# Optimization experiments

Measured on AMD Instinct MI355X. Metric: run time of the kernel, lower is better.

Reference implementation:

```python
import jax, jax.numpy as jnp
import numpy as np

B, M, N, DIM = 4, 3, 2048, 512
H = 4
HD = DIM // H  # 128
SCALE = float(np.sqrt(HD))  # code divides scores by sqrt(head_dim)


def setup_inputs() -> dict:
    key = jax.random.key(0)
    ks = jax.random.split(key, 9)
    s = 0.02
    return {
        "query": jax.random.normal(ks[0], (B, M, N, DIM), jnp.float32),
        "key": jax.random.normal(ks[1], (B, M, N, DIM), jnp.float32),
        "value": jax.random.normal(ks[2], (B, M, N, DIM), jnp.float32),
        "Wq": jax.random.normal(ks[3], (DIM, DIM), jnp.float32) * s,
        "bq": jax.random.normal(ks[4], (DIM,), jnp.float32) * s,
        "Wk": jax.random.normal(ks[5], (DIM, DIM), jnp.float32) * s,
        "bk": jax.random.normal(ks[6], (DIM,), jnp.float32) * s,
        "Wv": jax.random.normal(ks[7], (DIM, DIM), jnp.float32) * s,
        "bv": jax.random.normal(ks[8], (DIM,), jnp.float32) * s,
    }


def reference(query, key, value, Wq, bq, Wk, bk, Wv, bv):
    b, m, n, dim = query.shape
    # nn.Linear: x @ W.T + b
    Q = (query @ Wq.T + bq).reshape(b, m, n, H, HD)
    K = (key @ Wk.T + bk).reshape(b, m, n, H, HD)
    V = (value @ Wv.T + bv).reshape(b, m, n, H, HD)
    # scores: [b, m, H, n, n]
    scores = jnp.einsum("bmqhd,bmkhd->bmhqk", Q, K) / SCALE
    attn = jax.nn.softmax(scores, axis=-1)
    out = jnp.einsum("bmhqk,bmkhd->bmqhd", attn, V)
    return out.reshape(b, m, n, dim)
```

## Files before the change

kernel.cpp:

```cpp
#include <hip/hip_runtime.h>
#include <hip/hip_bf16.h>


typedef short s16x8 __attribute__((ext_vector_type(8)));
typedef unsigned short u16x8 __attribute__((ext_vector_type(8)));
typedef float f32x4 __attribute__((ext_vector_type(4)));

#define MFMA16(a, b, c) __builtin_amdgcn_mfma_f32_16x16x32_bf16((a), (b), (c), 0, 0, 0)

static __device__ __forceinline__ unsigned short f2bf(float f) {
    union { float f; unsigned u; } v; v.f = f;
    unsigned r = v.u + 0x7FFFu + ((v.u >> 16) & 1u);
    return (unsigned short)(r >> 16);
}
static __device__ __forceinline__ unsigned pk2(float a, float b) {
    unsigned r;
    asm("v_cvt_pk_bf16_f32 %0, %1, %2" : "=v"(r) : "v"(a), "v"(b));
    return r;
}

#define OSTR 72

__global__ __launch_bounds__(256, 2)
void qkv_proj_kernel(const float* __restrict__ Xq, const float* __restrict__ Xk,
                     const float* __restrict__ Xv,
                     const float* __restrict__ Wq, const float* __restrict__ bq,
                     const float* __restrict__ Wk, const float* __restrict__ bk,
                     const float* __restrict__ Wv, const float* __restrict__ bv,
                     unsigned short* __restrict__ ws_q,
                     unsigned short* __restrict__ ws_k,
                     unsigned short* __restrict__ ws_vt)
{
    __shared__ __align__(16) char smem[65536];

    const int which = blockIdx.z;
    const float* X    = (which == 0) ? Xq : (which == 1) ? Xk : Xv;
    const float* W    = (which == 0) ? Wq : (which == 1) ? Wk : Wv;
    const float* bias = (which == 0) ? bq : (which == 1) ? bk : bv;

    const int r0 = blockIdx.x * 128;
    const int c0 = blockIdx.y * 128;
    const int tid = threadIdx.x;
    const int lane = tid & 63, wave = tid >> 6;
    const int l15 = lane & 15, quad = lane >> 4;
    const int wr = (wave >> 1) * 64, wc = (wave & 1) * 64;

    const int srow = tid >> 4;
    const int scol = tid & 15;
    const int cf = scol * 4;
    const int cb = scol * 8;

    f32x4 acc[4][4] = {};

    {
        char* A0 = smem;
        char* B0 = smem + 16384;
        for (int i = 0; i < 8; ++i) {
            const int row = i * 16 + srow;
            float4 fa = *(const float4*)&X[(size_t)(r0 + row) * 512 + cf];
            float4 fb = *(const float4*)&W[(size_t)(c0 + row) * 512 + cf];
            uint2 wa, wb;
            wa.x = pk2(fa.x, fa.y); wa.y = pk2(fa.z, fa.w);
            wb.x = pk2(fb.x, fb.y); wb.y = pk2(fb.z, fb.w);
            const int sw = cb ^ ((row & 7) << 4);
            *(uint2*)(A0 + row * 128 + sw) = wa;
            *(uint2*)(B0 + row * 128 + sw) = wb;
        }
    }
    __syncthreads();

    for (int it = 0; it < 8; ++it) {
        char* Ac = smem + (it & 1) * 32768;
        char* Bc = Ac + 16384;
        const bool pre = (it < 7);

        float4 ra[8], rb[8];
        if (pre) {
            const int kn = (it + 1) * 64;
            for (int i = 0; i < 8; ++i) {
                const int row = i * 16 + srow;
                ra[i] = *(const float4*)&X[(size_t)(r0 + row) * 512 + kn + cf];
                rb[i] = *(const float4*)&W[(size_t)(c0 + row) * 512 + kn + cf];
            }
        }

        for (int kk = 0; kk < 2; ++kk) {
            s16x8 af[4], bf_[4];
            for (int mi = 0; mi < 4; ++mi) {
                const int row = wr + mi * 16 + l15;
                af[mi] = *(const s16x8*)(Ac + row * 128 +
                                         ((kk * 64 + quad * 16) ^ ((row & 7) << 4)));
            }
            for (int ni = 0; ni < 4; ++ni) {
                const int row = wc + ni * 16 + l15;
                bf_[ni] = *(const s16x8*)(Bc + row * 128 +
                                          ((kk * 64 + quad * 16) ^ ((row & 7) << 4)));
            }
            for (int mi = 0; mi < 4; ++mi)
                for (int ni = 0; ni < 4; ++ni)
                    acc[mi][ni] = MFMA16(af[mi], bf_[ni], acc[mi][ni]);
        }

        if (pre) {
            char* An = smem + ((it & 1) ^ 1) * 32768;
            char* Bn = An + 16384;
            for (int i = 0; i < 8; ++i) {
                const int row = i * 16 + srow;
                uint2 wa, wb;
                wa.x = pk2(ra[i].x, ra[i].y); wa.y = pk2(ra[i].z, ra[i].w);
                wb.x = pk2(rb[i].x, rb[i].y); wb.y = pk2(rb[i].z, rb[i].w);
                const int sw = cb ^ ((row & 7) << 4);
                *(uint2*)(An + row * 128 + sw) = wa;
                *(uint2*)(Bn + row * 128 + sw) = wb;
            }
        }
        __syncthreads();
    }

    float bvals[4];
    for (int ni = 0; ni < 4; ++ni) bvals[ni] = bias[c0 + wc + ni * 16 + l15];

    __syncthreads();
    unsigned short* St = (unsigned short*)smem + wave * (64 * OSTR);
    const int h = blockIdx.y;
    const int bm = (r0 + wr) >> 11;
    const int n0 = (r0 + wr) & 2047;

    if (which != 2) {
        for (int mi = 0; mi < 4; ++mi)
            for (int ni = 0; ni < 4; ++ni)
                for (int r = 0; r < 4; ++r)
                    St[(mi * 16 + quad * 4 + r) * OSTR + ni * 16 + l15] =
                        f2bf(acc[mi][ni][r] + bvals[ni]);
        unsigned short* dst = (which == 0) ? ws_q : ws_k;
        for (int p = 0; p < 8; ++p) {
            const int row = p * 8 + (lane >> 3);
            const int coff = (lane & 7) * 8;
            s16x8 v = *(const s16x8*)&St[row * OSTR + coff];
            *(s16x8*)&dst[((size_t)(bm * 4 + h) * 2048 + n0 + row) * 128 + wc + coff] = v;
        }
    } else {
        for (int mi = 0; mi < 4; ++mi)
            for (int ni = 0; ni < 4; ++ni)
                for (int r = 0; r < 4; ++r)
                    St[(ni * 16 + l15) * OSTR + mi * 16 + quad * 4 + r] =
                        f2bf(acc[mi][ni][r] + bvals[ni]);
        for (int p = 0; p < 8; ++p) {
            const int col = p * 8 + (lane >> 3);
            const int roff = (lane & 7) * 8;
            s16x8 v = *(const s16x8*)&St[col * OSTR + roff];
            *(s16x8*)&ws_vt[(((size_t)(bm * 4 + h)) * 128 + wc + col) * 2048 + n0 + roff] = v;
        }
    }
}

#define KSTR 272
#define VSTR 80
#define PQST 80

__global__ __launch_bounds__(256)
void attn_kernel(const unsigned short* __restrict__ Qw,
                 const unsigned short* __restrict__ Kw,
                 const unsigned short* __restrict__ Vtw,
                 float* __restrict__ out)
{
    __shared__ char lds[48128];
    char* Kb0 = lds;
    char* Kb1 = lds + 8704;
    char* Vb0 = lds + 17408;
    char* Vb1 = lds + 27648;
    char* Pb  = lds + 37888;

    const int tid = threadIdx.x, lane = tid & 63, wave = tid >> 6;
    const int l15 = lane & 15, quad = lane >> 4;
    const int q0 = blockIdx.x * 128, h = blockIdx.y, bm = blockIdx.z;

    const unsigned short* Qh = Qw  + (size_t)(bm * 4 + h) * 2048 * 128;
    const unsigned short* Kh = Kw  + (size_t)(bm * 4 + h) * 2048 * 128;
    const unsigned short* Vh = Vtw + (size_t)(bm * 4 + h) * 128 * 2048;

    const int sk_key  = tid >> 3, sk_c   = tid & 7;
    const int sv_hd   = tid >> 1, sv_hlf = tid & 1;

    s16x8 qf[2][4];
    for (int qh = 0; qh < 2; ++qh)
        for (int kk = 0; kk < 4; ++kk)
            qf[qh][kk] = *(const s16x8*)&Qh[(size_t)(q0 + wave * 32 + qh * 16 + l15) * 128 + kk * 32 + quad * 8];

    {
        u16x8 ka = *(const u16x8*)&Kh[(size_t)sk_key * 128 + sk_c * 16];
        u16x8 kb = *(const u16x8*)&Kh[(size_t)sk_key * 128 + sk_c * 16 + 8];
        u16x8 va = *(const u16x8*)&Vh[(size_t)sv_hd * 2048 + sv_hlf * 16];
        u16x8 vb = *(const u16x8*)&Vh[(size_t)sv_hd * 2048 + sv_hlf * 16 + 8];
        *(u16x8*)(Kb0 + sk_key * KSTR + sk_c * 32)      = ka;
        *(u16x8*)(Kb0 + sk_key * KSTR + sk_c * 32 + 16) = kb;
        *(u16x8*)(Vb0 + sv_hd * VSTR + sv_hlf * 32)      = va;
        *(u16x8*)(Vb0 + sv_hd * VSTR + sv_hlf * 32 + 16) = vb;
    }
    __syncthreads();

    f32x4 acc[2][8] = {};
    float rsum[2] = {0.f, 0.f};
    char* Pw = Pb + wave * 2560;

    const float CEXP = 1.4426950408889634f / 11.313708498984761f;

    for (int it = 0; it < 64; ++it) {
        const int k0 = it * 32;
        char* Kc = (it & 1) ? Kb1 : Kb0;
        char* Vc = (it & 1) ? Vb1 : Vb0;
        char* Kn = (it & 1) ? Kb0 : Kb1;
        char* Vn = (it & 1) ? Vb0 : Vb1;
        const bool do_stage = (it < 63);

        u16x8 ka, kb, va, vb;
        if (do_stage) {
            const int kn0 = k0 + 32;
            ka = *(const u16x8*)&Kh[(size_t)(kn0 + sk_key) * 128 + sk_c * 16];
            kb = *(const u16x8*)&Kh[(size_t)(kn0 + sk_key) * 128 + sk_c * 16 + 8];
            va = *(const u16x8*)&Vh[(size_t)sv_hd * 2048 + kn0 + sv_hlf * 16];
            vb = *(const u16x8*)&Vh[(size_t)sv_hd * 2048 + kn0 + sv_hlf * 16 + 8];
        }

        f32x4 s[2][2] = {};
        __builtin_amdgcn_s_setprio(1);
        for (int kk = 0; kk < 4; ++kk) {
            s16x8 kf0 = *(const s16x8*)(Kc + (l15)      * KSTR + (kk * 4 + quad) * 16);
            s16x8 kf1 = *(const s16x8*)(Kc + (16 + l15) * KSTR + (kk * 4 + quad) * 16);
            s[0][0] = MFMA16(kf0, qf[0][kk], s[0][0]);
            s[0][1] = MFMA16(kf1, qf[0][kk], s[0][1]);
            s[1][0] = MFMA16(kf0, qf[1][kk], s[1][0]);
            s[1][1] = MFMA16(kf1, qf[1][kk], s[1][1]);
        }
        __builtin_amdgcn_s_setprio(0);

        if (do_stage) {
            *(u16x8*)(Kn + sk_key * KSTR + sk_c * 32)      = ka;
            *(u16x8*)(Kn + sk_key * KSTR + sk_c * 32 + 16) = kb;
            *(u16x8*)(Vn + sv_hd * VSTR + sv_hlf * 32)      = va;
            *(u16x8*)(Vn + sv_hd * VSTR + sv_hlf * 32 + 16) = vb;
        }

        for (int qh = 0; qh < 2; ++qh)
            for (int ni = 0; ni < 2; ++ni) {
                const float p0 = exp2f(s[qh][ni][0] * CEXP);
                const float p1 = exp2f(s[qh][ni][1] * CEXP);
                const float p2 = exp2f(s[qh][ni][2] * CEXP);
                const float p3 = exp2f(s[qh][ni][3] * CEXP);
                rsum[qh] += (p0 + p1) + (p2 + p3);
                uint2 w; w.x = pk2(p0, p1); w.y = pk2(p2, p3);
                *(uint2*)(Pw + (qh * 16 + l15) * PQST + ni * 32 + quad * 8) = w;
            }

        s16x8 pf0 = *(const s16x8*)(Pw + (l15)      * PQST + quad * 16);
        s16x8 pf1 = *(const s16x8*)(Pw + (16 + l15) * PQST + quad * 16);
        __builtin_amdgcn_s_setprio(1);
        for (int mb = 0; mb < 8; ++mb) {
            s16x8 vtf = *(const s16x8*)(Vc + (mb * 16 + l15) * VSTR + quad * 16);
            acc[0][mb] = MFMA16(vtf, pf0, acc[0][mb]);
            acc[1][mb] = MFMA16(vtf, pf1, acc[1][mb]);
        }
        __builtin_amdgcn_s_setprio(0);

        __syncthreads();
    }

    for (int qh = 0; qh < 2; ++qh) {
        rsum[qh] += __shfl_xor(rsum[qh], 16);
        rsum[qh] += __shfl_xor(rsum[qh], 32);
    }
    for (int qh = 0; qh < 2; ++qh) {
        const float inv = 1.f / rsum[qh];
        float* orow = out + ((size_t)bm * 2048 + q0 + wave * 32 + qh * 16 + l15) * 512 + h * 128;
        for (int mb = 0; mb < 8; ++mb) {
            float4 v;
            v.x = acc[qh][mb][0] * inv; v.y = acc[qh][mb][1] * inv;
            v.z = acc[qh][mb][2] * inv; v.w = acc[qh][mb][3] * inv;
            *(float4*)&orow[mb * 16 + quad * 4] = v;
        }
    }
}

extern "C" void kernel_launch(void* const* d_in, const int* in_sizes, int n_in,
                              void* d_out, int out_size, void* d_ws, size_t ws_size,
                              hipStream_t stream) {
    const float* Xq = (const float*)d_in[0];
    const float* Xk = (const float*)d_in[1];
    const float* Xv = (const float*)d_in[2];
    const float* Wq = (const float*)d_in[3];
    const float* bq = (const float*)d_in[4];
    const float* Wk = (const float*)d_in[5];
    const float* bk = (const float*)d_in[6];
    const float* Wv = (const float*)d_in[7];
    const float* bv = (const float*)d_in[8];
    float* out = (float*)d_out;

    unsigned short* ws = (unsigned short*)d_ws;
    const size_t per_tensor = (size_t)12 * 4 * 2048 * 128;
    unsigned short* ws_q  = ws;
    unsigned short* ws_k  = ws + per_tensor;
    unsigned short* ws_vt = ws + 2 * per_tensor;

    qkv_proj_kernel<<<dim3(192, 4, 3), 256, 0, stream>>>(
        Xq, Xk, Xv, Wq, bq, Wk, bk, Wv, bv, ws_q, ws_k, ws_vt);

    attn_kernel<<<dim3(16, 4, 12), 256, 0, stream>>>(ws_q, ws_k, ws_vt, out);
}
```

Measured before the change: 447.4 us.

## Keep P in registers via permlane swaps, XOR-swizzle K in LDS, use hardware exp

Removes the per-wave LDS round trip for the probability tile. P is now packed into MFMA operand layout in registers using v_permlane32/16_swap, which saves LDS writes and reads and the LDS space they used. The padded K stride is replaced by an XOR swizzle to avoid bank conflicts without padding, and exp2f is replaced by raw v_exp_f32. The next-tile LDS stores move after the PV MFMAs, which delays them. The risks are that the permlane lane mapping must match the MFMA operand layout exactly, and that v_exp_f32 does no range handling.

```diff
diff --git a/kernel.cpp b/kernel.cpp
--- a/kernel.cpp
+++ b/kernel.cpp
@@ -16,6 +16,11 @@
 static __device__ __forceinline__ unsigned pk2(float a, float b) {
     unsigned r;
     asm("v_cvt_pk_bf16_f32 %0, %1, %2" : "=v"(r) : "v"(a), "v"(b));
+    return r;
+}
+static __device__ __forceinline__ float exp2_hw(float x) {
+    float r;
+    asm("v_exp_f32 %0, %1" : "=v"(r) : "v"(x));
     return r;
 }
 
@@ -154,9 +159,7 @@
     }
 }
 
-#define KSTR 272
 #define VSTR 80
-#define PQST 80
 
 __global__ __launch_bounds__(256)
 void attn_kernel(const unsigned short* __restrict__ Qw,
@@ -164,12 +167,11 @@
                  const unsigned short* __restrict__ Vtw,
                  float* __restrict__ out)
 {
-    __shared__ char lds[48128];
+    __shared__ char lds[36864];
     char* Kb0 = lds;
-    char* Kb1 = lds + 8704;
-    char* Vb0 = lds + 17408;
-    char* Vb1 = lds + 27648;
-    char* Pb  = lds + 37888;
+    char* Kb1 = lds + 8192;
+    char* Vb0 = lds + 16384;
+    char* Vb1 = lds + 26624;
 
     const int tid = threadIdx.x, lane = tid & 63, wave = tid >> 6;
     const int l15 = lane & 15, quad = lane >> 4;
@@ -181,6 +183,8 @@
 
     const int sk_key  = tid >> 3, sk_c   = tid & 7;
     const int sv_hd   = tid >> 1, sv_hlf = tid & 1;
+    const int skx = sk_key & 7;
+    const int krx = (l15 & 7) << 4;
 
     s16x8 qf[2][4];
     for (int qh = 0; qh < 2; ++qh)
@@ -192,8 +196,8 @@
         u16x8 kb = *(const u16x8*)&Kh[(size_t)sk_key * 128 + sk_c * 16 + 8];
         u16x8 va = *(const u16x8*)&Vh[(size_t)sv_hd * 2048 + sv_hlf * 16];
         u16x8 vb = *(const u16x8*)&Vh[(size_t)sv_hd * 2048 + sv_hlf * 16 + 8];
-        *(u16x8*)(Kb0 + sk_key * KSTR + sk_c * 32)      = ka;
-        *(u16x8*)(Kb0 + sk_key * KSTR + sk_c * 32 + 16) = kb;
+        *(u16x8*)(Kb0 + sk_key * 256 + (((sk_c * 2) ^ skx) << 4))     = ka;
+        *(u16x8*)(Kb0 + sk_key * 256 + (((sk_c * 2 + 1) ^ skx) << 4)) = kb;
         *(u16x8*)(Vb0 + sv_hd * VSTR + sv_hlf * 32)      = va;
         *(u16x8*)(Vb0 + sv_hd * VSTR + sv_hlf * 32 + 16) = vb;
     }
@@ -201,7 +205,6 @@
 
     f32x4 acc[2][8] = {};
     float rsum[2] = {0.f, 0.f};
-    char* Pw = Pb + wave * 2560;
 
     const float CEXP = 1.4426950408889634f / 11.313708498984761f;
 
@@ -225,8 +228,8 @@
         f32x4 s[2][2] = {};
         __builtin_amdgcn_s_setprio(1);
         for (int kk = 0; kk < 4; ++kk) {
-            s16x8 kf0 = *(const s16x8*)(Kc + (l15)      * KSTR + (kk * 4 + quad) * 16);
-            s16x8 kf1 = *(const s16x8*)(Kc + (16 + l15) * KSTR + (kk * 4 + quad) * 16);
+            s16x8 kf0 = *(const s16x8*)(Kc + l15 * 256        + (((kk * 4 + quad) << 4) ^ krx));
+            s16x8 kf1 = *(const s16x8*)(Kc + (16 + l15) * 256 + (((kk * 4 + quad) << 4) ^ krx));
             s[0][0] = MFMA16(kf0, qf[0][kk], s[0][0]);
             s[0][1] = MFMA16(kf1, qf[0][kk], s[0][1]);
             s[1][0] = MFMA16(kf0, qf[1][kk], s[1][0]);
@@ -234,33 +237,42 @@
         }
         __builtin_amdgcn_s_setprio(0);
 
-        if (do_stage) {
-            *(u16x8*)(Kn + sk_key * KSTR + sk_c * 32)      = ka;
-            *(u16x8*)(Kn + sk_key * KSTR + sk_c * 32 + 16) = kb;
-            *(u16x8*)(Vn + sv_hd * VSTR + sv_hlf * 32)      = va;
-            *(u16x8*)(Vn + sv_hd * VSTR + sv_hlf * 32 + 16) = vb;
-        }
-
-        for (int qh = 0; qh < 2; ++qh)
-            for (int ni = 0; ni < 2; ++ni) {
-                const float p0 = exp2f(s[qh][ni][0] * CEXP);
-                const float p1 = exp2f(s[qh][ni][1] * CEXP);
-                const float p2 = exp2f(s[qh][ni][2] * CEXP);
-                const float p3 = exp2f(s[qh][ni][3] * CEXP);
-                rsum[qh] += (p0 + p1) + (p2 + p3);
-                uint2 w; w.x = pk2(p0, p1); w.y = pk2(p2, p3);
-                *(uint2*)(Pw + (qh * 16 + l15) * PQST + ni * 32 + quad * 8) = w;
-            }
-
-        s16x8 pf0 = *(const s16x8*)(Pw + (l15)      * PQST + quad * 16);
-        s16x8 pf1 = *(const s16x8*)(Pw + (16 + l15) * PQST + quad * 16);
+        s16x8 pf[2];
+        for (int qh = 0; qh < 2; ++qh) {
+            const float p00 = exp2_hw(s[qh][0][0] * CEXP);
+            const float p01 = exp2_hw(s[qh][0][1] * CEXP);
+            const float p02 = exp2_hw(s[qh][0][2] * CEXP);
+            const float p03 = exp2_hw(s[qh][0][3] * CEXP);
+            const float p10 = exp2_hw(s[qh][1][0] * CEXP);
+            const float p11 = exp2_hw(s[qh][1][1] * CEXP);
+            const float p12 = exp2_hw(s[qh][1][2] * CEXP);
+            const float p13 = exp2_hw(s[qh][1][3] * CEXP);
+            rsum[qh] += ((p00 + p01) + (p02 + p03)) + ((p10 + p11) + (p12 + p13));
+            unsigned x0 = pk2(p00, p01), y0 = pk2(p02, p03);
+            unsigned x1 = pk2(p10, p11), y1 = pk2(p12, p13);
+            asm("v_permlane32_swap_b32 %0, %1" : "+v"(x0), "+v"(x1));
+            asm("v_permlane16_swap_b32 %0, %1" : "+v"(x0), "+v"(x1));
+            asm("v_permlane32_swap_b32 %0, %1" : "+v"(y0), "+v"(y1));
+            asm("v_permlane16_swap_b32 %0, %1" : "+v"(y0), "+v"(y1));
+            union { unsigned u[4]; s16x8 v; } pu;
+            pu.u[0] = x0; pu.u[1] = y0; pu.u[2] = x1; pu.u[3] = y1;
+            pf[qh] = pu.v;
+        }
+
         __builtin_amdgcn_s_setprio(1);
         for (int mb = 0; mb < 8; ++mb) {
             s16x8 vtf = *(const s16x8*)(Vc + (mb * 16 + l15) * VSTR + quad * 16);
-            acc[0][mb] = MFMA16(vtf, pf0, acc[0][mb]);
-            acc[1][mb] = MFMA16(vtf, pf1, acc[1][mb]);
+            acc[0][mb] = MFMA16(vtf, pf[0], acc[0][mb]);
+            acc[1][mb] = MFMA16(vtf, pf[1], acc[1][mb]);
         }
         __builtin_amdgcn_s_setprio(0);
+
+        if (do_stage) {
+            *(u16x8*)(Kn + sk_key * 256 + (((sk_c * 2) ^ skx) << 4))     = ka;
+            *(u16x8*)(Kn + sk_key * 256 + (((sk_c * 2 + 1) ^ skx) << 4)) = kb;
+            *(u16x8*)(Vn + sv_hd * VSTR + sv_hlf * 32)      = va;
+            *(u16x8*)(Vn + sv_hd * VSTR + sv_hlf * 32 + 16) = vb;
+        }
 
         __syncthreads();
     }
```

Measured after the change: 421.2 us. 5.8% less time.
